# Optimization experiments

Hardware: AMD Instinct MI355X
Metric: run time of the kernel (lower is better)

## Reference

```python
import jax, jax.numpy as jnp
import numpy as np

DIM = 768
NUM_HEADS = 12
HEAD_DIM = DIM // NUM_HEADS
SCALE = HEAD_DIM ** -0.5


def setup_inputs() -> dict:
    key = jax.random.key(0)
    k1, k2, k3, k4, k5 = jax.random.split(key, 5)
    B, N = 1, 4096
    x = jax.random.normal(k1, (B, N, DIM), dtype=jnp.float32)
    xpos = jax.random.randint(k2, (B, N, 2), 0, 64, dtype=jnp.int64)
    # learned parameters (torch nn.Linear convention: W is [out, in])
    W_qkv = jax.random.normal(k3, (3 * DIM, DIM), dtype=jnp.float32) * 0.02
    W_proj = jax.random.normal(k4, (DIM, DIM), dtype=jnp.float32) * 0.02
    b_proj = jax.random.normal(k5, (DIM,), dtype=jnp.float32) * 0.02
    return {"x": x, "xpos": xpos, "W_qkv": W_qkv, "W_proj": W_proj, "b_proj": b_proj}


def reference(x, xpos, W_qkv, W_proj, b_proj):
    B, N, C = x.shape
    H, D = NUM_HEADS, HEAD_DIM
    # qkv projection (no bias), then split into q,k,v of shape [B,H,N,D]
    qkv = jnp.einsum('bnc,fc->bnf', x, W_qkv)            # [B,N,3C]
    qkv = qkv.reshape(B, N, 3, H, D).transpose(2, 0, 3, 1, 4)  # [3,B,H,N,D]
    q, k, v = qkv[0], qkv[1], qkv[2]
    # rope is None in this config -> q,k unchanged; xpos unused
    attn = jnp.einsum('bhnd,bhmd->bhnm', q, k) * SCALE   # [B,H,N,N]
    attn = jax.nn.softmax(attn, axis=-1)
    out = jnp.einsum('bhnm,bhmd->bhnd', attn, v)          # [B,H,N,D]
    out = out.transpose(0, 2, 1, 3).reshape(B, N, C)      # [B,N,C]
    out = jnp.einsum('bnc,oc->bno', out, W_proj) + b_proj
    return out
```

## Files before the change

### kernel.cpp

```cpp
#include <hip/hip_runtime.h>

#define DEVI __device__ __forceinline__

typedef unsigned short u16;
typedef unsigned int u32;
using u16x8 = __attribute__((ext_vector_type(8))) u16;
using u16x4 = __attribute__((ext_vector_type(4))) u16;
using u32x4 = __attribute__((ext_vector_type(4))) u32;
using bf16x8 = __attribute__((ext_vector_type(8))) __bf16;
using f32x4 = __attribute__((ext_vector_type(4))) float;
using f32x16 = __attribute__((ext_vector_type(16))) float;

typedef const __attribute__((address_space(1))) u32 gu32;
typedef __attribute__((address_space(3))) u32 lu32;

#if __has_builtin(__builtin_amdgcn_exp2f)
#define EXP2(x) __builtin_amdgcn_exp2f(x)
#else
#define EXP2(x) __builtin_exp2f(x)
#endif

DEVI u16 f2bf(float f) {
    u32 u = __builtin_bit_cast(u32, f);
    u32 r = (u + 0x7fffu + ((u >> 16) & 1u)) >> 16;
    return (u16)r;
}
DEVI float bf2f(u16 b) {
    u32 u = ((u32)b) << 16;
    return __builtin_bit_cast(float, u);
}
DEVI u32 cvtpk_bf16(float lo, float hi) {
    u32 r;
    asm("v_cvt_pk_bf16_f32 %0, %1, %2" : "=v"(r) : "v"(lo), "v"(hi));
    return r;
}

DEVI bf16x8 frag_ld(const u16* p) {
    return __builtin_bit_cast(bf16x8, *(const u16x8*)p);
}

DEVI void async16(const void* g, void* lds) {
    __builtin_amdgcn_global_load_lds((gu32*)g, (lu32*)lds, 16, 0, 0);
}

#define MFMA32(a, b, c) __builtin_amdgcn_mfma_f32_32x32x16_bf16(a, b, c, 0, 0, 0)

#define QK_SCALE 0.18033688011112042f

__global__ void cvt3_kernel(const float* __restrict__ s0, const float* __restrict__ s1,
                            const float* __restrict__ s2,
                            u16* __restrict__ d0, u16* __restrict__ d1, u16* __restrict__ d2,
                            int n0, int n1) {
    int i = (blockIdx.x * blockDim.x + threadIdx.x) * 4;
    const float* s; u16* d;
    if (i < n0) { s = s0; d = d0; }
    else if (i < n0 + n1) { s = s1 - n0; d = d1 - n0; }
    else { s = s2 - (n0 + n1); d = d2 - (n0 + n1); }
    float4 v = *(const float4*)(s + i);
    u16x4 o;
    o[0] = f2bf(v.x); o[1] = f2bf(v.y); o[2] = f2bf(v.z); o[3] = f2bf(v.w);
    *(u16x4*)(d + i) = o;
}

template<int MODE>
__global__ __launch_bounds__(256) void gemm_bt(const u16* __restrict__ A,
                                               const u16* __restrict__ B,
                                               void* __restrict__ Out,
                                               const float* __restrict__ bias,
                                               int M, int Nn, int K) {
    const int m0 = blockIdx.x * 128, n0 = blockIdx.y * 128;
    const int tid = threadIdx.x, w = tid >> 6, lane = tid & 63;
    const int l15 = lane & 15, l4 = lane >> 4;
    __shared__ __align__(16) u16 As[128 * 32];
    __shared__ __align__(16) u16 Bs[128 * 32];
    const int wm = (w >> 1) * 64, wn = (w & 1) * 64;
    f32x4 acc[4][4] = {};
    const int srow = lane >> 2;
    const int sk = (lane & 3) * 8;

    for (int kt = 0; kt < K; kt += 32) {
#pragma unroll
        for (int it = 0; it < 2; ++it) {
            const int rbase = (w * 2 + it) * 16;
            async16(A + (size_t)(m0 + rbase + srow) * K + kt + sk, &As[rbase * 32]);
            async16(B + (size_t)(n0 + rbase + srow) * K + kt + sk, &Bs[rbase * 32]);
        }
        __syncthreads();
        bf16x8 af[4], bfr[4];
#pragma unroll
        for (int i = 0; i < 4; ++i) {
            af[i] = frag_ld(&As[(wm + i * 16 + l15) * 32 + l4 * 8]);
            bfr[i] = frag_ld(&Bs[(wn + i * 16 + l15) * 32 + l4 * 8]);
        }
#pragma unroll
        for (int i = 0; i < 4; ++i)
#pragma unroll
            for (int j = 0; j < 4; ++j)
                acc[i][j] = __builtin_amdgcn_mfma_f32_16x16x32_bf16(af[i], bfr[j], acc[i][j], 0, 0, 0);
        __syncthreads();
    }
#pragma unroll
    for (int i = 0; i < 4; ++i)
#pragma unroll
        for (int j = 0; j < 4; ++j)
#pragma unroll
            for (int r = 0; r < 4; ++r) {
                const int row = m0 + wm + i * 16 + l4 * 4 + r;
                const int col = n0 + wn + j * 16 + l15;
                if (MODE == 0) {
                    float v = acc[i][j][r];
                    if (col < 768) v *= QK_SCALE;
                    ((u16*)Out)[(size_t)row * Nn + col] = f2bf(v);
                } else {
                    ((float*)Out)[(size_t)row * Nn + col] = acc[i][j][r] + bias[col];
                }
            }
}

__global__ __launch_bounds__(256) void pack_kv(const u16* __restrict__ qkv,
                                               u16* __restrict__ kt,
                                               u16* __restrict__ vt2) {
    const int sb = blockIdx.x;
    const int h = blockIdx.y;
    const int tid = threadIdx.x;
    __shared__ u16 T[64][72];
#pragma unroll
    for (int rd = 0; rd < 2; ++rd) {
        const int idx = rd * 256 + tid;
        const int row = idx >> 3, ch = idx & 7;
        u16x8 v = *(const u16x8*)(qkv + (size_t)(sb * 64 + row) * 2304 + 1536 + h * 64 + ch * 8);
        *(u16x8*)&T[row][ch * 8] = v;
    }
#pragma unroll
    for (int rd = 0; rd < 2; ++rd) {
        const int o = rd * 256 + tid;
        const int s_loc = o >> 8, mm = (o >> 6) & 3, lane = o & 63;
        const int l31 = lane & 31, hi = lane >> 5;
        u16x8 kv = *(const u16x8*)(qkv + (size_t)(sb * 64 + s_loc * 32 + l31) * 2304 +
                                   768 + h * 64 + mm * 16 + hi * 8);
        const int s = sb * 2 + s_loc;
        *(u16x8*)(kt + ((size_t)(h * 128 + s) * 4 + mm) * 512 + lane * 8) = kv;
    }
    __syncthreads();
#pragma unroll
    for (int rd = 0; rd < 2; ++rd) {
        const int o = rd * 256 + tid;
        const int s_loc = o >> 8, f = (o >> 6) & 3, lane = o & 63;
        const int ks = f >> 1, Oh = f & 1;
        const int l31 = lane & 31, hi = lane >> 5;
        u16x8 ov;
#pragma unroll
        for (int j = 0; j < 8; ++j) {
            const int kvloc = 32 * s_loc + 16 * ks + (j & 3) + 8 * (j >> 2) + 4 * hi;
            ov[j] = T[kvloc][Oh * 32 + l31];
        }
        const int s = sb * 2 + s_loc;
        *(u16x8*)(vt2 + ((size_t)(h * 128 + s) * 4 + f) * 512 + lane * 8) = ov;
    }
}

__global__ __launch_bounds__(256, 4) void attn_kernel(const u16* __restrict__ qkv,
                                                      const u16* __restrict__ kt,
                                                      const u16* __restrict__ vt2,
                                                      u16* __restrict__ op,
                                                      float* __restrict__ lsums) {
    const int id = blockIdx.x;
    const int xcd = id & 7, slot = id >> 3;
    const int gi = slot >> 5, qbi = slot & 31;
    const int g = gi * 8 + xcd;
    const int h = g % 12, sp = g / 12;
    const int tid = threadIdx.x, w = tid >> 6, lane = tid & 63;
    const int l31 = lane & 31, hi = lane >> 5;
    const int q0 = qbi * 128 + w * 32;

    bf16x8 qf0, qf1, qf2, qf3;
    {
        const u16* qp = qkv + (size_t)(q0 + l31) * 2304 + h * 64 + hi * 8;
        qf0 = frag_ld(qp); qf1 = frag_ld(qp + 16);
        qf2 = frag_ld(qp + 32); qf3 = frag_ld(qp + 48);
    }

    const u16* kc = kt + (size_t)(h * 128 + sp * 32) * 2048 + lane * 8;
    const u16* vc = vt2 + (size_t)(h * 128 + sp * 32) * 2048 + lane * 8;

    f32x16 O0 = {}, O1 = {};
    float lsum = 0.f;

    bf16x8 kf0 = frag_ld(kc), kf1 = frag_ld(kc + 512),
           kf2 = frag_ld(kc + 1024), kf3 = frag_ld(kc + 1536);
    bf16x8 vf0 = frag_ld(vc), vf1 = frag_ld(vc + 512),
           vf2 = frag_ld(vc + 1024), vf3 = frag_ld(vc + 1536);
    kc += 2048; vc += 2048;

#pragma unroll 1
    for (int s = 0; s < 32; ++s) {
        f32x16 S = {};
        __builtin_amdgcn_s_setprio(1);
        S = MFMA32(kf0, qf0, S);
        S = MFMA32(kf1, qf1, S);
        S = MFMA32(kf2, qf2, S);
        S = MFMA32(kf3, qf3, S);
        __builtin_amdgcn_s_setprio(0);
        kf0 = frag_ld(kc); kf1 = frag_ld(kc + 512);
        kf2 = frag_ld(kc + 1024); kf3 = frag_ld(kc + 1536);
        kc += 2048;

        float e[16];
#pragma unroll
        for (int r = 0; r < 16; ++r) e[r] = EXP2(S[r]);
        u32x4 w0 = { cvtpk_bf16(e[0], e[1]), cvtpk_bf16(e[2], e[3]),
                     cvtpk_bf16(e[4], e[5]), cvtpk_bf16(e[6], e[7]) };
        u32x4 w1 = { cvtpk_bf16(e[8], e[9]), cvtpk_bf16(e[10], e[11]),
                     cvtpk_bf16(e[12], e[13]), cvtpk_bf16(e[14], e[15]) };
        bf16x8 pas0 = __builtin_bit_cast(bf16x8, w0);
        bf16x8 pas1 = __builtin_bit_cast(bf16x8, w1);
        lsum += ((((e[0] + e[1]) + (e[2] + e[3])) +
                  ((e[4] + e[5]) + (e[6] + e[7]))) +
                 (((e[8] + e[9]) + (e[10] + e[11])) +
                  ((e[12] + e[13]) + (e[14] + e[15]))));

        __builtin_amdgcn_s_setprio(1);
        O0 = MFMA32(pas0, vf0, O0);
        O1 = MFMA32(pas0, vf1, O1);
        O0 = MFMA32(pas1, vf2, O0);
        O1 = MFMA32(pas1, vf3, O1);
        __builtin_amdgcn_s_setprio(0);
        vf0 = frag_ld(vc); vf1 = frag_ld(vc + 512);
        vf2 = frag_ld(vc + 1024); vf3 = frag_ld(vc + 1536);
        vc += 2048;
    }

    lsum += __shfl_xor(lsum, 32);
    u16* ob = op + (size_t)sp * 3145728;
    const int rr4 = 4 * hi;
#pragma unroll
    for (int r = 0; r < 16; ++r) {
        const int q = (r & 3) + 8 * (r >> 2) + rr4;
        const size_t rowoff = (size_t)(q0 + q) * 768 + h * 64 + l31;
        ob[rowoff] = f2bf(O0[r]);
        ob[rowoff + 32] = f2bf(O1[r]);
    }
    if (hi == 0)
        lsums[(size_t)sp * 49152 + (size_t)(q0 + l31) * 12 + h] = lsum;
}

__global__ __launch_bounds__(256) void combine_kernel(const u16* __restrict__ op,
                                                      const float* __restrict__ lsums,
                                                      u16* __restrict__ outb) {
    const int gid = blockIdx.x * 256 + threadIdx.x;
    const int e = gid * 8;
    const int q = e / 768, c = e % 768, h = c >> 6;
    float lt = 0.f;
#pragma unroll
    for (int sp = 0; sp < 4; ++sp) lt += lsums[(size_t)sp * 49152 + q * 12 + h];
    const float inv = 1.0f / lt;
    float acc[8] = {};
#pragma unroll
    for (int sp = 0; sp < 4; ++sp) {
        u16x8 o = *(const u16x8*)(op + (size_t)sp * 3145728 + (size_t)q * 768 + c);
#pragma unroll
        for (int jj = 0; jj < 8; ++jj) acc[jj] += bf2f(o[jj]);
    }
    u16x8 o;
#pragma unroll
    for (int jj = 0; jj < 8; ++jj) o[jj] = f2bf(acc[jj] * inv);
    *(u16x8*)(outb + e) = o;
}

extern "C" void kernel_launch(void* const* d_in, const int* in_sizes, int n_in,
                              void* d_out, int out_size, void* d_ws, size_t ws_size,
                              hipStream_t stream) {
    const float* x = (const float*)d_in[0];
    const float* Wqkv = (const float*)d_in[2];
    const float* Wproj = (const float*)d_in[3];
    const float* bproj = (const float*)d_in[4];

    u16* ws = (u16*)d_ws;
    u16* x_bf = ws;
    u16* wqkv_bf = x_bf + 3145728;
    u16* wproj_bf = wqkv_bf + 1769472;
    u16* qkv = wproj_bf + 589824;
    u16* attn_bf = qkv + 9437184;
    u16* vt2 = attn_bf + 3145728;
    u16* o_part = vt2 + 3145728;
    float* lsums = (float*)(o_part + 12582912);
    u16* kt = x_bf;

    cvt3_kernel<<<5376, 256, 0, stream>>>(x, Wqkv, Wproj, x_bf, wqkv_bf, wproj_bf,
                                          3145728, 1769472);

    gemm_bt<0><<<dim3(32, 18), 256, 0, stream>>>(x_bf, wqkv_bf, qkv, nullptr, 4096, 2304, 768);
    pack_kv<<<dim3(64, 12), 256, 0, stream>>>(qkv, kt, vt2);
    attn_kernel<<<1536, 256, 0, stream>>>(qkv, kt, vt2, o_part, lsums);
    combine_kernel<<<1536, 256, 0, stream>>>(o_part, lsums, attn_bf);
    gemm_bt<1><<<dim3(32, 6), 256, 0, stream>>>(attn_bf, wproj_bf, d_out, bproj, 4096, 768, 768);
}
```

Baseline: 133.8 us.

## Process two 32-query tiles per wave to reuse K/V fragments

Each attention block now runs 2 waves instead of 4, and each wave handles 64 queries as two 32-row tiles that share the same K and V fragments loaded from global memory. This halves K/V fragment loads per query and interleaves independent MFMA chains to improve issue overlap. In exchange it doubles the accumulator and score registers per wave and lowers the waves per block and the launch-bounds occupancy hint, so latency hiding may suffer.

```diff
diff --git a/kernel.cpp b/kernel.cpp
--- a/kernel.cpp
+++ b/kernel.cpp
@@ -159,7 +159,7 @@
     }
 }
 
-__global__ __launch_bounds__(256, 4) void attn_kernel(const u16* __restrict__ qkv,
+__global__ __launch_bounds__(128, 2) void attn_kernel(const u16* __restrict__ qkv,
                                                       const u16* __restrict__ kt,
                                                       const u16* __restrict__ vt2,
                                                       u16* __restrict__ op,
@@ -171,20 +171,23 @@
     const int h = g % 12, sp = g / 12;
     const int tid = threadIdx.x, w = tid >> 6, lane = tid & 63;
     const int l31 = lane & 31, hi = lane >> 5;
-    const int q0 = qbi * 128 + w * 32;
-
-    bf16x8 qf0, qf1, qf2, qf3;
+    const int q0 = qbi * 128 + w * 64;
+
+    bf16x8 qA0, qA1, qA2, qA3, qB0, qB1, qB2, qB3;
     {
         const u16* qp = qkv + (size_t)(q0 + l31) * 2304 + h * 64 + hi * 8;
-        qf0 = frag_ld(qp); qf1 = frag_ld(qp + 16);
-        qf2 = frag_ld(qp + 32); qf3 = frag_ld(qp + 48);
+        qA0 = frag_ld(qp); qA1 = frag_ld(qp + 16);
+        qA2 = frag_ld(qp + 32); qA3 = frag_ld(qp + 48);
+        const u16* qp2 = qp + (size_t)32 * 2304;
+        qB0 = frag_ld(qp2); qB1 = frag_ld(qp2 + 16);
+        qB2 = frag_ld(qp2 + 32); qB3 = frag_ld(qp2 + 48);
     }
 
     const u16* kc = kt + (size_t)(h * 128 + sp * 32) * 2048 + lane * 8;
     const u16* vc = vt2 + (size_t)(h * 128 + sp * 32) * 2048 + lane * 8;
 
-    f32x16 O0 = {}, O1 = {};
-    float lsum = 0.f;
+    f32x16 O0 = {}, O1 = {}, O2 = {}, O3 = {};
+    float lsumA = 0.f, lsumB = 0.f;
 
     bf16x8 kf0 = frag_ld(kc), kf1 = frag_ld(kc + 512),
            kf2 = frag_ld(kc + 1024), kf3 = frag_ld(kc + 1536);
@@ -194,43 +197,56 @@
 
 #pragma unroll 1
     for (int s = 0; s < 32; ++s) {
-        f32x16 S = {};
+        f32x16 S0 = {}, S1 = {};
         __builtin_amdgcn_s_setprio(1);
-        S = MFMA32(kf0, qf0, S);
-        S = MFMA32(kf1, qf1, S);
-        S = MFMA32(kf2, qf2, S);
-        S = MFMA32(kf3, qf3, S);
+        S0 = MFMA32(kf0, qA0, S0);  S1 = MFMA32(kf0, qB0, S1);
+        S0 = MFMA32(kf1, qA1, S0);  S1 = MFMA32(kf1, qB1, S1);
+        S0 = MFMA32(kf2, qA2, S0);  S1 = MFMA32(kf2, qB2, S1);
+        S0 = MFMA32(kf3, qA3, S0);  S1 = MFMA32(kf3, qB3, S1);
         __builtin_amdgcn_s_setprio(0);
         kf0 = frag_ld(kc); kf1 = frag_ld(kc + 512);
         kf2 = frag_ld(kc + 1024); kf3 = frag_ld(kc + 1536);
         kc += 2048;
 
-        float e[16];
-#pragma unroll
-        for (int r = 0; r < 16; ++r) e[r] = EXP2(S[r]);
-        u32x4 w0 = { cvtpk_bf16(e[0], e[1]), cvtpk_bf16(e[2], e[3]),
-                     cvtpk_bf16(e[4], e[5]), cvtpk_bf16(e[6], e[7]) };
-        u32x4 w1 = { cvtpk_bf16(e[8], e[9]), cvtpk_bf16(e[10], e[11]),
-                     cvtpk_bf16(e[12], e[13]), cvtpk_bf16(e[14], e[15]) };
-        bf16x8 pas0 = __builtin_bit_cast(bf16x8, w0);
-        bf16x8 pas1 = __builtin_bit_cast(bf16x8, w1);
-        lsum += ((((e[0] + e[1]) + (e[2] + e[3])) +
-                  ((e[4] + e[5]) + (e[6] + e[7]))) +
-                 (((e[8] + e[9]) + (e[10] + e[11])) +
-                  ((e[12] + e[13]) + (e[14] + e[15]))));
+        float e[16], f[16];
+#pragma unroll
+        for (int r = 0; r < 16; ++r) e[r] = EXP2(S0[r]);
+#pragma unroll
+        for (int r = 0; r < 16; ++r) f[r] = EXP2(S1[r]);
+        u32x4 wa0 = { cvtpk_bf16(e[0], e[1]), cvtpk_bf16(e[2], e[3]),
+                      cvtpk_bf16(e[4], e[5]), cvtpk_bf16(e[6], e[7]) };
+        u32x4 wa1 = { cvtpk_bf16(e[8], e[9]), cvtpk_bf16(e[10], e[11]),
+                      cvtpk_bf16(e[12], e[13]), cvtpk_bf16(e[14], e[15]) };
+        u32x4 wb0 = { cvtpk_bf16(f[0], f[1]), cvtpk_bf16(f[2], f[3]),
+                      cvtpk_bf16(f[4], f[5]), cvtpk_bf16(f[6], f[7]) };
+        u32x4 wb1 = { cvtpk_bf16(f[8], f[9]), cvtpk_bf16(f[10], f[11]),
+                      cvtpk_bf16(f[12], f[13]), cvtpk_bf16(f[14], f[15]) };
+        bf16x8 pasA0 = __builtin_bit_cast(bf16x8, wa0);
+        bf16x8 pasA1 = __builtin_bit_cast(bf16x8, wa1);
+        bf16x8 pasB0 = __builtin_bit_cast(bf16x8, wb0);
+        bf16x8 pasB1 = __builtin_bit_cast(bf16x8, wb1);
+        lsumA += ((((e[0] + e[1]) + (e[2] + e[3])) +
+                   ((e[4] + e[5]) + (e[6] + e[7]))) +
+                  (((e[8] + e[9]) + (e[10] + e[11])) +
+                   ((e[12] + e[13]) + (e[14] + e[15]))));
+        lsumB += ((((f[0] + f[1]) + (f[2] + f[3])) +
+                   ((f[4] + f[5]) + (f[6] + f[7]))) +
+                  (((f[8] + f[9]) + (f[10] + f[11])) +
+                   ((f[12] + f[13]) + (f[14] + f[15]))));
 
         __builtin_amdgcn_s_setprio(1);
-        O0 = MFMA32(pas0, vf0, O0);
-        O1 = MFMA32(pas0, vf1, O1);
-        O0 = MFMA32(pas1, vf2, O0);
-        O1 = MFMA32(pas1, vf3, O1);
+        O0 = MFMA32(pasA0, vf0, O0);  O2 = MFMA32(pasB0, vf0, O2);
+        O1 = MFMA32(pasA0, vf1, O1);  O3 = MFMA32(pasB0, vf1, O3);
+        O0 = MFMA32(pasA1, vf2, O0);  O2 = MFMA32(pasB1, vf2, O2);
+        O1 = MFMA32(pasA1, vf3, O1);  O3 = MFMA32(pasB1, vf3, O3);
         __builtin_amdgcn_s_setprio(0);
         vf0 = frag_ld(vc); vf1 = frag_ld(vc + 512);
         vf2 = frag_ld(vc + 1024); vf3 = frag_ld(vc + 1536);
         vc += 2048;
     }
 
-    lsum += __shfl_xor(lsum, 32);
+    lsumA += __shfl_xor(lsumA, 32);
+    lsumB += __shfl_xor(lsumB, 32);
     u16* ob = op + (size_t)sp * 3145728;
     const int rr4 = 4 * hi;
 #pragma unroll
@@ -239,9 +255,14 @@
         const size_t rowoff = (size_t)(q0 + q) * 768 + h * 64 + l31;
         ob[rowoff] = f2bf(O0[r]);
         ob[rowoff + 32] = f2bf(O1[r]);
-    }
-    if (hi == 0)
-        lsums[(size_t)sp * 49152 + (size_t)(q0 + l31) * 12 + h] = lsum;
+        const size_t rowoff2 = rowoff + (size_t)32 * 768;
+        ob[rowoff2] = f2bf(O2[r]);
+        ob[rowoff2 + 32] = f2bf(O3[r]);
+    }
+    if (hi == 0) {
+        lsums[(size_t)sp * 49152 + (size_t)(q0 + l31) * 12 + h] = lsumA;
+        lsums[(size_t)sp * 49152 + (size_t)(q0 + 32 + l31) * 12 + h] = lsumB;
+    }
 }
 
 __global__ __launch_bounds__(256) void combine_kernel(const u16* __restrict__ op,
@@ -291,7 +312,7 @@
 
     gemm_bt<0><<<dim3(32, 18), 256, 0, stream>>>(x_bf, wqkv_bf, qkv, nullptr, 4096, 2304, 768);
     pack_kv<<<dim3(64, 12), 256, 0, stream>>>(qkv, kt, vt2);
-    attn_kernel<<<1536, 256, 0, stream>>>(qkv, kt, vt2, o_part, lsums);
+    attn_kernel<<<1536, 128, 0, stream>>>(qkv, kt, vt2, o_part, lsums);
     combine_kernel<<<1536, 256, 0, stream>>>(o_part, lsums, attn_bf);
     gemm_bt<1><<<dim3(32, 6), 256, 0, stream>>>(attn_bf, wproj_bf, d_out, bproj, 4096, 768, 768);
 }
```

Measured after the change: 127.8 us. -4.5%, faster.
